# Kernel tuning notes

Measured on AMD Instinct MI355X. Metric: run time of the kernel, lower is better.

The kernel has to match this reference:

```python
import jax, jax.numpy as jnp
import numpy as np

B, L, H = 64, 512, 768

def setup_inputs() -> dict:
    key = jax.random.key(0)
    k1, k2, k3, k4 = jax.random.split(key, 4)
    scale = 1.0 / np.sqrt(H)
    return {
        "hidden_states": jax.random.normal(k1, (B, L, H), dtype=jnp.float32),
        "W_fc": jax.random.normal(k2, (H, H), dtype=jnp.float32) * scale,
        "b_fc": jax.random.normal(k3, (H,), dtype=jnp.float32) * scale,
        "W_nu": jax.random.normal(k4, (H,), dtype=jnp.float32) * scale,
    }

def reference(hidden_states, W_fc, b_fc, W_nu):
    # upsilon = tanh(Linear(hidden_states)); [B, L, H]
    upsilon = jnp.tanh(jnp.einsum("blh,hk->blk", hidden_states, W_fc.T) + b_fc)
    # per-token attention logits: [B, L]  (replaces per-sample torch.mv loop)
    nu = jnp.einsum("blh,h->bl", upsilon, W_nu)
    alphas = jax.nn.softmax(nu, axis=1)
    # weighted-sum pooling: [B, H]  (replaces per-sample torch.mm loop)
    pooled = jnp.einsum("bl,blh->bh", alphas, hidden_states)
    return pooled
```

## Files before the change

### kernel.cpp

```cpp
#include <hip/hip_runtime.h>

#define H_DIM 768
#define B_DIM 64
#define L_DIM 512
#define M_TOT (B_DIM*L_DIM)
#define BM 128
#define BN 128
#define BK 64
#define NB_CNT (H_DIM/BN)
#define KB_CNT (H_DIM/BK)
#define MB_CNT (M_TOT/BM)
#define TILE_HALFS (BM*BK)
#define BUFH 16384

typedef _Float16 f16x8 __attribute__((ext_vector_type(8)));
typedef float f32x4 __attribute__((ext_vector_type(4)));

#define WS_W16   0u
#define WS_NUP   1179648u
#define WS_ALPHA 1966080u
#define WS_POOL  2097152u
#define WS_AIMG  3670016u
#define WS_NEED_IMG (WS_AIMG + (size_t)M_TOT*H_DIM*2)

__device__ __forceinline__ void gload_lds16(const void* g, void* l) {
  __builtin_amdgcn_global_load_lds((const __attribute__((address_space(1))) void*)g,
                                   (__attribute__((address_space(3))) void*)l, 16, 0, 0);
}

__device__ __forceinline__ f16x8 cvt8(const float* src) {
  f32x4 x0 = *(const f32x4*)src;
  f32x4 x1 = *(const f32x4*)(src + 4);
  f16x8 h;
  h[0]=(_Float16)x0[0]; h[1]=(_Float16)x0[1]; h[2]=(_Float16)x0[2]; h[3]=(_Float16)x0[3];
  h[4]=(_Float16)x1[0]; h[5]=(_Float16)x1[1]; h[6]=(_Float16)x1[2]; h[7]=(_Float16)x1[3];
  return h;
}

__device__ __forceinline__ float fast_tanh(float v) {
  float e = __builtin_amdgcn_exp2f(v * 2.8853900817779268f);
  return 1.0f - 2.0f * __builtin_amdgcn_rcpf(e + 1.0f);
}

#define SBAR()  do { __builtin_amdgcn_sched_barrier(0); \
                     __builtin_amdgcn_s_barrier(); \
                     __builtin_amdgcn_sched_barrier(0); } while (0)

__global__ __launch_bounds__(256) void conv_kernel(const float* __restrict__ Wfc,
                                                   const float* __restrict__ hs,
                                                   _Float16* __restrict__ W16,
                                                   _Float16* __restrict__ Aimg) {
  int t = blockIdx.x;
  const float* srcb;
  _Float16* dstb;
  if (t < NB_CNT * KB_CNT) {
    int nb = t / KB_CNT, kb = t % KB_CNT;
    srcb = Wfc + (size_t)(nb*BN)*H_DIM + kb*BK;
    dstb = W16 + (size_t)t*TILE_HALFS;
  } else {
    int u = t - NB_CNT * KB_CNT;
    int mb = u / KB_CNT, kb = u % KB_CNT;
    srcb = hs + (size_t)(mb*BM)*H_DIM + kb*BK;
    dstb = Aimg + (size_t)u*TILE_HALFS;
  }
#pragma unroll
  for (int i = 0; i < 4; ++i) {
    int u = threadIdx.x + i * 256;
    int row = u >> 3, sp = u & 7;
    int sl = sp ^ (row & 7);
    *(f16x8*)(dstb + u*8) = cvt8(srcb + (size_t)row*H_DIM + sl*8);
  }
}

__device__ __forceinline__ void stage128(const _Float16* at, const _Float16* wt,
                                         _Float16* Lb, int tid) {
#pragma unroll
  for (int i = 0; i < 4; ++i) {
    int e = (tid + i*256) * 8;
    gload_lds16(at + e, Lb + e);
  }
#pragma unroll
  for (int i = 0; i < 4; ++i) {
    int e = (tid + i*256) * 8;
    gload_lds16(wt + e, Lb + 8192 + e);
  }
}

__device__ __forceinline__ void rd_frags(const _Float16* base, const int aoff[4],
                                         const int boff[4], int slot,
                                         f16x8 af[4], f16x8 bf[4]) {
#pragma unroll
  for (int mi = 0; mi < 4; ++mi) af[mi] = *(const f16x8*)(base + aoff[mi] + slot);
#pragma unroll
  for (int ni = 0; ni < 4; ++ni) bf[ni] = *(const f16x8*)(base + boff[ni] + slot);
}

__device__ __forceinline__ void mfma16(const f16x8 af[4], const f16x8 bf[4],
                                       f32x4 acc[4][4]) {
  __builtin_amdgcn_s_setprio(1);
#pragma unroll
  for (int mi = 0; mi < 4; ++mi)
#pragma unroll
    for (int ni = 0; ni < 4; ++ni)
      acc[mi][ni] = __builtin_amdgcn_mfma_f32_16x16x32_f16(af[mi], bf[ni], acc[mi][ni], 0, 0, 0);
  __builtin_amdgcn_s_setprio(0);
}

__global__ __launch_bounds__(256, 2) void gemm_nu_img_kernel(const _Float16* __restrict__ Aimg,
                                                             const _Float16* __restrict__ W16,
                                                             const float* __restrict__ bfc,
                                                             const float* __restrict__ wnu,
                                                             float* __restrict__ nup) {
  __shared__ __align__(16) _Float16 LS[2 * BUFH];
  __shared__ float nred[2][BM];

  int bid = blockIdx.x;
  int mb = bid & (MB_CNT - 1);
  int nb = bid >> 8;
  int m0 = mb * BM, n0 = nb * BN;
  int tid = threadIdx.x;
  int wv = tid >> 6, ln = tid & 63;
  int wr = wv >> 1, wc = wv & 1;
  int lrow = ln & 15, lk = ln >> 4;

  f32x4 acc[4][4] = {};
  f16x8 af0[4], bf0[4], af1[4], bf1[4];
  const _Float16* abase = Aimg + (size_t)(mb * KB_CNT) * TILE_HALFS;
  const _Float16* wbase = W16  + (size_t)(nb * KB_CNT) * TILE_HALFS;
  _Float16* b0 = LS;
  _Float16* b1 = LS + BUFH;

  int aoff[4], boff[4];
#pragma unroll
  for (int mi = 0; mi < 4; ++mi) aoff[mi] = (wr*64 + mi*16 + lrow) * 64;
#pragma unroll
  for (int ni = 0; ni < 4; ++ni) boff[ni] = 8192 + (wc*64 + ni*16 + lrow) * 64;
  int slot0 = ((0*4 + lk) ^ (lrow & 7)) * 8;
  int slot1 = ((1*4 + lk) ^ (lrow & 7)) * 8;

  float wn[4], bb[4];
#pragma unroll
  for (int ni = 0; ni < 4; ++ni) {
    int c = n0 + wc*64 + ni*16 + lrow;
    wn[ni] = wnu[c];
    bb[ni] = bfc[c];
  }
  asm volatile("" :: "v"(wn[0]), "v"(wn[1]), "v"(wn[2]), "v"(wn[3]),
                     "v"(bb[0]), "v"(bb[1]), "v"(bb[2]), "v"(bb[3]));
  asm volatile("s_waitcnt vmcnt(0)" ::: "memory");

  stage128(abase,              wbase,              b0, tid);
  stage128(abase + TILE_HALFS, wbase + TILE_HALFS, b1, tid);
  asm volatile("s_waitcnt vmcnt(8)" ::: "memory");
  SBAR();
  rd_frags(b0, aoff, boff, slot0, af0, bf0);

#pragma unroll 1
  for (int kt2 = 0; kt2 < 5; ++kt2) {
    const _Float16* a2 = abase + (size_t)(kt2*2 + 2) * TILE_HALFS;
    const _Float16* w2 = wbase + (size_t)(kt2*2 + 2) * TILE_HALFS;
    const _Float16* a3 = abase + (size_t)(kt2*2 + 3) * TILE_HALFS;
    const _Float16* w3 = wbase + (size_t)(kt2*2 + 3) * TILE_HALFS;
    rd_frags(b0, aoff, boff, slot1, af1, bf1);
    mfma16(af0, bf0, acc);
    asm volatile("s_waitcnt lgkmcnt(0)" ::: "memory");
    SBAR();
    stage128(a2, w2, b0, tid);
    asm volatile("s_waitcnt vmcnt(8)" ::: "memory");
    SBAR();
    rd_frags(b1, aoff, boff, slot0, af0, bf0);
    mfma16(af1, bf1, acc);
    rd_frags(b1, aoff, boff, slot1, af1, bf1);
    mfma16(af0, bf0, acc);
    asm volatile("s_waitcnt lgkmcnt(0)" ::: "memory");
    SBAR();
    stage128(a3, w3, b1, tid);
    asm volatile("s_waitcnt vmcnt(8)" ::: "memory");
    SBAR();
    rd_frags(b0, aoff, boff, slot0, af0, bf0);
    mfma16(af1, bf1, acc);
  }

  rd_frags(b0, aoff, boff, slot1, af1, bf1);
  mfma16(af0, bf0, acc);
  asm volatile("s_waitcnt vmcnt(0)" ::: "memory");
  SBAR();
  rd_frags(b1, aoff, boff, slot0, af0, bf0);
  mfma16(af1, bf1, acc);
  rd_frags(b1, aoff, boff, slot1, af1, bf1);
  mfma16(af0, bf0, acc);
  mfma16(af1, bf1, acc);

#pragma unroll
  for (int mi = 0; mi < 4; ++mi) {
#pragma unroll
    for (int r = 0; r < 4; ++r) {
      float s = 0.f;
#pragma unroll
      for (int ni = 0; ni < 4; ++ni)
        s = fmaf(fast_tanh(acc[mi][ni][r] + bb[ni]), wn[ni], s);
      for (int o = 1; o < 16; o <<= 1) s += __shfl_xor(s, o, 64);
      if (lrow == 0) nred[wc][wr*64 + mi*16 + lk*4 + r] = s;
    }
  }
  __syncthreads();
  if (tid < BM)
    nup[(size_t)nb * M_TOT + m0 + tid] = nred[0][tid] + nred[1][tid];
}

__global__ __launch_bounds__(256) void gemm_nu_kernel(const float* __restrict__ A,
                                                      const _Float16* __restrict__ W16,
                                                      const float* __restrict__ bfc,
                                                      const float* __restrict__ wnu,
                                                      float* __restrict__ nup) {
  __shared__ __align__(16) _Float16 lsA[TILE_HALFS];
  __shared__ __align__(16) _Float16 lsB[TILE_HALFS];
  __shared__ float nred[2][BM];

  int bid = blockIdx.x;
  int nb = bid % NB_CNT;
  int mb = bid / NB_CNT;
  int m0 = mb * BM, n0 = nb * BN;
  int tid = threadIdx.x;
  int wv = tid >> 6, ln = tid & 63;
  int wr = wv >> 1, wc = wv & 1;
  int lrow = ln & 15, lk = ln >> 4;

  f32x4 acc[4][4] = {};
  const _Float16* wbase = W16 + (size_t)(nb * KB_CNT) * TILE_HALFS;

  for (int kb = 0; kb < KB_CNT; ++kb) {
    const _Float16* wt = wbase + (size_t)kb * TILE_HALFS;
    for (int i = 0; i < 4; ++i) {
      int e = (tid + i*256) * 8;
      gload_lds16(wt + e, lsB + e);
    }
    for (int i = 0; i < 4; ++i) {
      int u = tid + i * 256;
      int row = u >> 3, sl = u & 7;
      *(f16x8*)(lsA + row*BK + ((sl ^ (row & 7)) * 8)) =
          cvt8(A + (size_t)(m0 + row) * H_DIM + kb*BK + sl*8);
    }
    __syncthreads();
#pragma unroll
    for (int kk = 0; kk < 2; ++kk) {
      f16x8 af[4], bf[4];
      int s = kk*4 + lk;
#pragma unroll
      for (int mi = 0; mi < 4; ++mi) {
        int r = wr*64 + mi*16 + lrow;
        af[mi] = *(const f16x8*)(lsA + r*BK + ((s ^ (r & 7)) * 8));
      }
#pragma unroll
      for (int ni = 0; ni < 4; ++ni) {
        int r = wc*64 + ni*16 + lrow;
        bf[ni] = *(const f16x8*)(lsB + r*BK + ((s ^ (r & 7)) * 8));
      }
#pragma unroll
      for (int mi = 0; mi < 4; ++mi)
#pragma unroll
        for (int ni = 0; ni < 4; ++ni)
          acc[mi][ni] = __builtin_amdgcn_mfma_f32_16x16x32_f16(af[mi], bf[ni], acc[mi][ni], 0, 0, 0);
    }
    __syncthreads();
  }

  float wn[4], bb[4];
  for (int ni = 0; ni < 4; ++ni) {
    int c = n0 + wc*64 + ni*16 + lrow;
    wn[ni] = wnu[c];
    bb[ni] = bfc[c];
  }
  for (int mi = 0; mi < 4; ++mi) {
    for (int r = 0; r < 4; ++r) {
      float s = 0.f;
      for (int ni = 0; ni < 4; ++ni)
        s = fmaf(fast_tanh(acc[mi][ni][r] + bb[ni]), wn[ni], s);
      for (int o = 1; o < 16; o <<= 1) s += __shfl_xor(s, o, 64);
      if (lrow == 0) nred[wc][wr*64 + mi*16 + lk*4 + r] = s;
    }
  }
  __syncthreads();
  if (tid < BM)
    nup[(size_t)nb * M_TOT + m0 + tid] = nred[0][tid] + nred[1][tid];
}

__global__ __launch_bounds__(512) void softmax_kernel(const float* __restrict__ nup,
                                                      float* __restrict__ alphas) {
  int b = blockIdx.x;
  int l = threadIdx.x;
  int m = b * L_DIM + l;
  float v = 0.f;
  for (int nb = 0; nb < NB_CNT; ++nb) v += nup[(size_t)nb * M_TOT + m];
  __shared__ float smax[8], ssum[8];
  int w = l >> 6, ln = l & 63;
  float mx = v;
  for (int o = 1; o < 64; o <<= 1) mx = fmaxf(mx, __shfl_xor(mx, o, 64));
  if (ln == 0) smax[w] = mx;
  __syncthreads();
  mx = smax[0];
  for (int i = 1; i < 8; ++i) mx = fmaxf(mx, smax[i]);
  float e = __expf(v - mx);
  float sm = e;
  for (int o = 1; o < 64; o <<= 1) sm += __shfl_xor(sm, o, 64);
  if (ln == 0) ssum[w] = sm;
  __syncthreads();
  float tot = 0.f;
  for (int i = 0; i < 8; ++i) tot += ssum[i];
  alphas[m] = e / tot;
}

__global__ __launch_bounds__(192) void pool1_img_kernel(const _Float16* __restrict__ img,
                                                        const float* __restrict__ alphas,
                                                        float* __restrict__ part) {
  int b = blockIdx.x >> 3;
  int lc = blockIdx.x & 7;
  int tid = threadIdx.x;
  int g = tid % 96, rp = tid / 96;
  int kb = g >> 3, sl = g & 7;
  __shared__ float al[64];
  __shared__ float tmp[2][H_DIM];
  if (tid < 64) al[tid] = alphas[b * L_DIM + lc*64 + tid];
  __syncthreads();
  float s[8] = {};
  for (int l = rp; l < 64; l += 2) {
    int m = b * L_DIM + lc*64 + l;
    int mb = m >> 7, row = m & 127;
    const f16x8* src = (const f16x8*)(img + ((size_t)(mb*KB_CNT + kb))*TILE_HALFS
                                      + row*64 + ((sl ^ (row & 7)) * 8));
    f16x8 h = *src;
    float a = al[l];
#pragma unroll
    for (int j = 0; j < 8; ++j) s[j] = fmaf(a, (float)h[j], s[j]);
  }
#pragma unroll
  for (int j = 0; j < 8; ++j) tmp[rp][g*8 + j] = s[j];
  __syncthreads();
  float* dst = part + ((size_t)lc * B_DIM + b) * H_DIM + tid*4;
  f32x4 o;
#pragma unroll
  for (int q = 0; q < 4; ++q) o[q] = tmp[0][tid*4 + q] + tmp[1][tid*4 + q];
  *(f32x4*)dst = o;
}

__global__ __launch_bounds__(256) void pool1_kernel(const float* __restrict__ hs,
                                                    const float* __restrict__ alphas,
                                                    float* __restrict__ part) {
  int b = blockIdx.x >> 3;
  int lc = blockIdx.x & 7;
  int tid = threadIdx.x;
  __shared__ float al[64];
  if (tid < 64) al[tid] = alphas[b * L_DIM + lc*64 + tid];
  __syncthreads();
  const float* xp = hs + ((size_t)b * L_DIM + lc*64) * H_DIM;
  int h0 = tid * 3;
  float s0 = 0.f, s1 = 0.f, s2 = 0.f;
  for (int l = 0; l < 64; ++l) {
    float a = al[l];
    const float* r = xp + (size_t)l * H_DIM + h0;
    s0 += a * r[0]; s1 += a * r[1]; s2 += a * r[2];
  }
  float* dst = part + ((size_t)lc * B_DIM + b) * H_DIM + h0;
  dst[0] = s0; dst[1] = s1; dst[2] = s2;
}

__global__ __launch_bounds__(256) void pool2_kernel(const float* __restrict__ part,
                                                    float* __restrict__ out) {
  int i = blockIdx.x * 256 + threadIdx.x;
  float s = 0.f;
  for (int lc = 0; lc < 8; ++lc) s += part[(size_t)lc * (B_DIM * H_DIM) + i];
  out[i] = s;
}

extern "C" void kernel_launch(void* const* d_in, const int* in_sizes, int n_in,
                              void* d_out, int out_size, void* d_ws, size_t ws_size,
                              hipStream_t stream) {
  const float* hs  = (const float*)d_in[0];
  const float* Wfc = (const float*)d_in[1];
  const float* bfc = (const float*)d_in[2];
  const float* wnu = (const float*)d_in[3];
  float* out = (float*)d_out;
  char* ws = (char*)d_ws;
  _Float16* W16 = (_Float16*)(ws + WS_W16);
  float* nup    = (float*)(ws + WS_NUP);
  float* alphas = (float*)(ws + WS_ALPHA);
  float* part   = (float*)(ws + WS_POOL);

  bool img = (ws_size >= WS_NEED_IMG);
  _Float16* Aimg = (_Float16*)(ws + WS_AIMG);
  if (img) {
    conv_kernel<<<(NB_CNT + MB_CNT) * KB_CNT, 256, 0, stream>>>(Wfc, hs, W16, Aimg);
    gemm_nu_img_kernel<<<MB_CNT * NB_CNT, 256, 0, stream>>>(Aimg, W16, bfc, wnu, nup);
  } else {
    conv_kernel<<<NB_CNT * KB_CNT, 256, 0, stream>>>(Wfc, hs, W16, Aimg);
    gemm_nu_kernel<<<MB_CNT * NB_CNT, 256, 0, stream>>>(hs, W16, bfc, wnu, nup);
  }
  softmax_kernel<<<B_DIM, 512, 0, stream>>>(nup, alphas);
  if (img) {
    pool1_img_kernel<<<B_DIM * 8, 192, 0, stream>>>(Aimg, alphas, part);
  } else {
    pool1_kernel<<<B_DIM * 8, 256, 0, stream>>>(hs, alphas, part);
  }
  pool2_kernel<<<192, 256, 0, stream>>>(part, out);
}
```

Baseline: 98.52 us.

## Make each GEMM block handle three N-tiles with a continuous staging pipeline

Each GEMM block now processes three consecutive 128-column N-tiles instead of one, so the grid shrinks from 1536 to 512 blocks. The double-buffered staging continues across N-tile boundaries: the next tile's first K-slices are prefetched while the current tile finishes. The epilogue reduction is rewritten to go through a padded LDS scratch array instead of shuffle reductions. This cuts per-block prologue/drain overhead and keeps the MFMA pipeline busy across tiles. In exchange it uses fewer blocks, which can hurt load balance and occupancy, and adds extra barriers in each epilogue.

Result: faster. 91.83 us (-6.8%).

```diff
diff --git a/kernel.cpp b/kernel.cpp
--- a/kernel.cpp
+++ b/kernel.cpp
@@ -106,18 +106,75 @@
   __builtin_amdgcn_s_setprio(0);
 }
 
+#define PASS_ITER(P, j) do {                                                   \
+    _Float16* bufc_ = ((j) & 1) ? b1 : b0;                                     \
+    _Float16* bufn_ = ((j) & 1) ? b0 : b1;                                     \
+    rd_frags(bufc_, aoff, boff, slot1, af1, bf1);                              \
+    mfma16(af0, bf0, acc);                                                     \
+    asm volatile("s_waitcnt lgkmcnt(0)" ::: "memory");                         \
+    SBAR();                                                                    \
+    if ((P) < 2 || (j) < 10) {                                                 \
+      const _Float16* aS = abase + (size_t)(((j) < 10) ? (j) + 2 : (j) - 10) * TILE_HALFS; \
+      stage128(aS, wS, bufc_, tid);                                            \
+      wS += TILE_HALFS;                                                        \
+    }                                                                          \
+    if ((P) == 2 && (j) == 10) { asm volatile("s_waitcnt vmcnt(0)" ::: "memory"); } \
+    else                       { asm volatile("s_waitcnt vmcnt(8)" ::: "memory"); } \
+    SBAR();                                                                    \
+    rd_frags(bufn_, aoff, boff, slot0, af0, bf0);                              \
+    mfma16(af1, bf1, acc);                                                     \
+  } while (0)
+
+#define EPI(P) do {                                                            \
+    float s16_[4][4];                                                          \
+    _Pragma("unroll") for (int mi = 0; mi < 4; ++mi)                           \
+    _Pragma("unroll") for (int r = 0; r < 4; ++r) {                            \
+      float s_ = 0.f;                                                          \
+      _Pragma("unroll") for (int ni = 0; ni < 4; ++ni)                         \
+        s_ = fmaf(fast_tanh(acc[mi][ni][r] + bb[P][ni]), wn[P][ni], s_);       \
+      s16_[mi][r] = s_;                                                        \
+    }                                                                          \
+    if (wc == 0) {                                                             \
+      _Pragma("unroll") for (int mi = 0; mi < 4; ++mi)                         \
+      _Pragma("unroll") for (int r = 0; r < 4; ++r)                            \
+        scr[(wr*64 + mi*16 + lk*4 + r)*20 + lrow] = s16_[mi][r];               \
+    }                                                                          \
+    asm volatile("s_waitcnt lgkmcnt(0)" ::: "memory");                         \
+    SBAR();                                                                    \
+    float pa_ = 0.f;                                                           \
+    if (tid < 128) {                                                           \
+      const f32x4* sp_ = (const f32x4*)(scr + tid*20);                         \
+      f32x4 q_ = sp_[0] + sp_[1] + sp_[2] + sp_[3];                            \
+      pa_ = q_[0] + q_[1] + q_[2] + q_[3];                                     \
+    }                                                                          \
+    asm volatile("s_waitcnt lgkmcnt(0)" ::: "memory");                         \
+    SBAR();                                                                    \
+    if (wc == 1) {                                                             \
+      _Pragma("unroll") for (int mi = 0; mi < 4; ++mi)                         \
+      _Pragma("unroll") for (int r = 0; r < 4; ++r)                            \
+        scr[(wr*64 + mi*16 + lk*4 + r)*20 + lrow] = s16_[mi][r];               \
+    }                                                                          \
+    asm volatile("s_waitcnt lgkmcnt(0)" ::: "memory");                         \
+    SBAR();                                                                    \
+    if (tid < 128) {                                                           \
+      const f32x4* sp_ = (const f32x4*)(scr + tid*20);                         \
+      f32x4 q_ = sp_[0] + sp_[1] + sp_[2] + sp_[3];                            \
+      nup[(size_t)(nb0 + (P)) * M_TOT + m0 + tid] = pa_ + q_[0]+q_[1]+q_[2]+q_[3]; \
+    }                                                                          \
+  } while (0)
+
 __global__ __launch_bounds__(256, 2) void gemm_nu_img_kernel(const _Float16* __restrict__ Aimg,
                                                              const _Float16* __restrict__ W16,
                                                              const float* __restrict__ bfc,
                                                              const float* __restrict__ wnu,
                                                              float* __restrict__ nup) {
   __shared__ __align__(16) _Float16 LS[2 * BUFH];
-  __shared__ float nred[2][BM];
+  __shared__ __align__(16) float scr[128 * 20];
 
   int bid = blockIdx.x;
   int mb = bid & (MB_CNT - 1);
-  int nb = bid >> 8;
-  int m0 = mb * BM, n0 = nb * BN;
+  int nb0 = (bid >> 8) * 3;
+  int m0 = mb * BM;
   int tid = threadIdx.x;
   int wv = tid >> 6, ln = tid & 63;
   int wr = wv >> 1, wc = wv & 1;
@@ -126,7 +183,7 @@
   f32x4 acc[4][4] = {};
   f16x8 af0[4], bf0[4], af1[4], bf1[4];
   const _Float16* abase = Aimg + (size_t)(mb * KB_CNT) * TILE_HALFS;
-  const _Float16* wbase = W16  + (size_t)(nb * KB_CNT) * TILE_HALFS;
+  const _Float16* wbase = W16  + (size_t)(nb0 * KB_CNT) * TILE_HALFS;
   _Float16* b0 = LS;
   _Float16* b1 = LS + BUFH;
 
@@ -138,74 +195,46 @@
   int slot0 = ((0*4 + lk) ^ (lrow & 7)) * 8;
   int slot1 = ((1*4 + lk) ^ (lrow & 7)) * 8;
 
-  float wn[4], bb[4];
-#pragma unroll
-  for (int ni = 0; ni < 4; ++ni) {
-    int c = n0 + wc*64 + ni*16 + lrow;
-    wn[ni] = wnu[c];
-    bb[ni] = bfc[c];
-  }
-  asm volatile("" :: "v"(wn[0]), "v"(wn[1]), "v"(wn[2]), "v"(wn[3]),
-                     "v"(bb[0]), "v"(bb[1]), "v"(bb[2]), "v"(bb[3]));
+  float wn[3][4], bb[3][4];
+#pragma unroll
+  for (int p = 0; p < 3; ++p)
+#pragma unroll
+    for (int ni = 0; ni < 4; ++ni) {
+      int c = (nb0 + p)*BN + wc*64 + ni*16 + lrow;
+      wn[p][ni] = wnu[c];
+      bb[p][ni] = bfc[c];
+    }
   asm volatile("s_waitcnt vmcnt(0)" ::: "memory");
 
   stage128(abase,              wbase,              b0, tid);
   stage128(abase + TILE_HALFS, wbase + TILE_HALFS, b1, tid);
+  const _Float16* wS = wbase + 2 * TILE_HALFS;
   asm volatile("s_waitcnt vmcnt(8)" ::: "memory");
   SBAR();
   rd_frags(b0, aoff, boff, slot0, af0, bf0);
 
 #pragma unroll 1
-  for (int kt2 = 0; kt2 < 5; ++kt2) {
-    const _Float16* a2 = abase + (size_t)(kt2*2 + 2) * TILE_HALFS;
-    const _Float16* w2 = wbase + (size_t)(kt2*2 + 2) * TILE_HALFS;
-    const _Float16* a3 = abase + (size_t)(kt2*2 + 3) * TILE_HALFS;
-    const _Float16* w3 = wbase + (size_t)(kt2*2 + 3) * TILE_HALFS;
-    rd_frags(b0, aoff, boff, slot1, af1, bf1);
-    mfma16(af0, bf0, acc);
-    asm volatile("s_waitcnt lgkmcnt(0)" ::: "memory");
-    SBAR();
-    stage128(a2, w2, b0, tid);
-    asm volatile("s_waitcnt vmcnt(8)" ::: "memory");
-    SBAR();
-    rd_frags(b1, aoff, boff, slot0, af0, bf0);
-    mfma16(af1, bf1, acc);
-    rd_frags(b1, aoff, boff, slot1, af1, bf1);
-    mfma16(af0, bf0, acc);
-    asm volatile("s_waitcnt lgkmcnt(0)" ::: "memory");
-    SBAR();
-    stage128(a3, w3, b1, tid);
-    asm volatile("s_waitcnt vmcnt(8)" ::: "memory");
-    SBAR();
-    rd_frags(b0, aoff, boff, slot0, af0, bf0);
-    mfma16(af1, bf1, acc);
-  }
-
-  rd_frags(b0, aoff, boff, slot1, af1, bf1);
-  mfma16(af0, bf0, acc);
-  asm volatile("s_waitcnt vmcnt(0)" ::: "memory");
-  SBAR();
-  rd_frags(b1, aoff, boff, slot0, af0, bf0);
-  mfma16(af1, bf1, acc);
+  for (int j = 0; j < 12; ++j) PASS_ITER(0, j);
+  EPI(0);
+#pragma unroll
+  for (int mi = 0; mi < 4; ++mi)
+#pragma unroll
+    for (int ni = 0; ni < 4; ++ni) acc[mi][ni] = f32x4{0.f, 0.f, 0.f, 0.f};
+
+#pragma unroll 1
+  for (int j = 0; j < 12; ++j) PASS_ITER(1, j);
+  EPI(1);
+#pragma unroll
+  for (int mi = 0; mi < 4; ++mi)
+#pragma unroll
+    for (int ni = 0; ni < 4; ++ni) acc[mi][ni] = f32x4{0.f, 0.f, 0.f, 0.f};
+
+#pragma unroll 1
+  for (int j = 0; j < 11; ++j) PASS_ITER(2, j);
   rd_frags(b1, aoff, boff, slot1, af1, bf1);
   mfma16(af0, bf0, acc);
   mfma16(af1, bf1, acc);
-
-#pragma unroll
-  for (int mi = 0; mi < 4; ++mi) {
-#pragma unroll
-    for (int r = 0; r < 4; ++r) {
-      float s = 0.f;
-#pragma unroll
-      for (int ni = 0; ni < 4; ++ni)
-        s = fmaf(fast_tanh(acc[mi][ni][r] + bb[ni]), wn[ni], s);
-      for (int o = 1; o < 16; o <<= 1) s += __shfl_xor(s, o, 64);
-      if (lrow == 0) nred[wc][wr*64 + mi*16 + lk*4 + r] = s;
-    }
-  }
-  __syncthreads();
-  if (tid < BM)
-    nup[(size_t)nb * M_TOT + m0 + tid] = nred[0][tid] + nred[1][tid];
+  EPI(2);
 }
 
 __global__ __launch_bounds__(256) void gemm_nu_kernel(const float* __restrict__ A,
@@ -390,7 +419,7 @@
   _Float16* Aimg = (_Float16*)(ws + WS_AIMG);
   if (img) {
     conv_kernel<<<(NB_CNT + MB_CNT) * KB_CNT, 256, 0, stream>>>(Wfc, hs, W16, Aimg);
-    gemm_nu_img_kernel<<<MB_CNT * NB_CNT, 256, 0, stream>>>(Aimg, W16, bfc, wnu, nup);
+    gemm_nu_img_kernel<<<MB_CNT * 2, 256, 0, stream>>>(Aimg, W16, bfc, wnu, nup);
   } else {
     conv_kernel<<<NB_CNT * KB_CNT, 256, 0, stream>>>(Wfc, hs, W16, Aimg);
     gemm_nu_kernel<<<MB_CNT * NB_CNT, 256, 0, stream>>>(hs, W16, bfc, wnu, nup);
```
